# Performance work log

Measured on AMD Instinct MI355X. Metric: run time of the kernel, lower is better.

Reference implementation:

```python
import jax, jax.numpy as jnp
import numpy as np
from jax import lax

N, T, H = 16, 2048, 512


def setup_inputs() -> dict:
    key = jax.random.key(0)
    ks = jax.random.split(key, 4)
    scale = 0.02  # keep gates/tanh out of hard saturation
    return {
        "x": jax.random.normal(ks[0], (N, T, H), dtype=jnp.float32),
        "hidden": jnp.zeros((N, H), dtype=jnp.float32),
        "Wq": jax.random.normal(ks[1], (H, 2 * H), dtype=jnp.float32) * scale,
        "bq": jnp.zeros((H,), dtype=jnp.float32),
        "Wk": jax.random.normal(ks[2], (H, 2 * H), dtype=jnp.float32) * scale,
        "bk": jnp.zeros((H,), dtype=jnp.float32),
        "Wv": jax.random.normal(ks[3], (H, 2 * H), dtype=jnp.float32) * scale,
        "bv": jnp.zeros((H,), dtype=jnp.float32),
    }


def reference(x, hidden, Wq, bq, Wk, bk, Wv, bv):
    # x: (N, T, H); hidden: (N, H). torch Linear: y = cat @ W.T + b
    def step(h, xt):
        cat = jnp.concatenate([xt, h], axis=-1)  # (N, 2H)
        q = cat @ Wq.T + bq
        k = cat @ Wk.T + bk
        v = cat @ Wv.T + bv
        w = jax.nn.sigmoid(q * k)
        h_new = (1.0 - w) * h + w * jnp.tanh(v)
        return h_new, h  # emit PRE-update hidden (matches torch append-before-update)

    xs = jnp.swapaxes(x, 0, 1)  # (T, N, H)
    h_final, hiddens = lax.scan(step, hidden, xs)
    return jnp.swapaxes(hiddens, 0, 1), h_final  # (N, T, H), (N, H)
```

## Files before the change

### kernel.cpp

```cpp
#include <hip/hip_runtime.h>

#define N_B 16
#define T_S 2048
#define H_D 512
#define TH_F ((size_t)T_S * H_D)
#define NTH ((size_t)N_B * TH_F)
#define NGROUP 8
#define WPG 32
#define THREADS 512

#define STASH(dst, src) asm volatile("v_accvgpr_write_b32 %0, %1" : "=a"(dst) : "v"(src))
#define FETCH(dst, src) asm volatile("v_accvgpr_read_b32 %0, %1" : "=v"(dst) : "a"(src))

__global__ __launch_bounds__(THREADS, 1) void rnn_persist(
    const float* __restrict__ x,
    const float* __restrict__ hidden,
    const float* __restrict__ Wq, const float* __restrict__ bq,
    const float* __restrict__ Wk, const float* __restrict__ bk,
    const float* __restrict__ Wv, const float* __restrict__ bv,
    float* __restrict__ out,
    int* __restrict__ cnt)
{
    const int tid  = threadIdx.x;
    const int lane = tid & 63;
    const int wv   = tid >> 6;
    const int g    = blockIdx.x & 7;
    const int wm   = blockIdx.x >> 3;
    const int b0 = 2 * g, b1 = 2 * g + 1;
    const int jA = wm * 16 + 2 * wv;

    __shared__ __align__(16) float hs[2][H_D];

    float awx[2][3][8], awh[2][3][8];
    #pragma unroll
    for (int r = 0; r < 2; ++r) {
        const int j = jA + r;
        #pragma unroll
        for (int m = 0; m < 3; ++m) {
            const float* W = (m == 0) ? Wq : (m == 1) ? Wk : Wv;
            const float* base = W + (size_t)j * 1024 + lane * 8;
            float4 x0 = *(const float4*)(base);
            float4 x1 = *(const float4*)(base + 4);
            float4 h0 = *(const float4*)(base + 512);
            float4 h1 = *(const float4*)(base + 516);
            STASH(awx[r][m][0], x0.x); STASH(awx[r][m][1], x0.y);
            STASH(awx[r][m][2], x0.z); STASH(awx[r][m][3], x0.w);
            STASH(awx[r][m][4], x1.x); STASH(awx[r][m][5], x1.y);
            STASH(awx[r][m][6], x1.z); STASH(awx[r][m][7], x1.w);
            STASH(awh[r][m][0], h0.x); STASH(awh[r][m][1], h0.y);
            STASH(awh[r][m][2], h0.z); STASH(awh[r][m][3], h0.w);
            STASH(awh[r][m][4], h1.x); STASH(awh[r][m][5], h1.y);
            STASH(awh[r][m][6], h1.z); STASH(awh[r][m][7], h1.w);
        }
    }

    const int jw = jA + ((lane >> 1) & 1);
    const int bw = (lane & 1) ? b1 : b0;
    const float bqw = bq[jw], bkw = bk[jw], bvw = bv[jw];
    float ho = hidden[bw * H_D + jw];

    const int h_nb  = tid >> 8;
    const int u     = tid & 255;
    const int h_pos = u * 2;
    const int h_b   = h_nb ? b1 : b0;

    {
        float v0 = hidden[h_b * H_D + h_pos];
        float v1 = hidden[h_b * H_D + h_pos + 1];
        *(float2*)&hs[h_nb][h_pos] = make_float2(v0, v1);
        if (wm == 0) {
            out[(size_t)h_b * TH_F + h_pos]     = v0;
            out[(size_t)h_b * TH_F + h_pos + 1] = v1;
        }
    }
    __syncthreads();

    const float4* xb0 = (const float4*)(x + (size_t)b0 * TH_F) + lane * 2;
    const float4* xb1 = (const float4*)(x + (size_t)b1 * TH_F) + lane * 2;
    float ax[2][8];
    {
        float4 a = xb0[0], b = xb0[1], c = xb1[0], d = xb1[1];
        ax[0][0]=a.x; ax[0][1]=a.y; ax[0][2]=a.z; ax[0][3]=a.w;
        ax[0][4]=b.x; ax[0][5]=b.y; ax[0][6]=b.z; ax[0][7]=b.w;
        ax[1][0]=c.x; ax[1][1]=c.y; ax[1][2]=c.z; ax[1][3]=c.w;
        ax[1][4]=d.x; ax[1][5]=d.y; ax[1][6]=d.z; ax[1][7]=d.w;
    }

    int* mycnt = cnt + g * 64;

    for (int t = 0; t < T_S; ++t) {
        const bool do_next = (t + 1 < T_S);

        float acc[2][3][2];
        #pragma unroll
        for (int r = 0; r < 2; ++r)
            #pragma unroll
            for (int m = 0; m < 3; ++m) {
                float wreg[8];
                #pragma unroll
                for (int c = 0; c < 8; ++c) FETCH(wreg[c], awx[r][m][c]);
                float s0 = 0.f, s1 = 0.f;
                #pragma unroll
                for (int c = 0; c < 8; ++c) {
                    s0 = fmaf(wreg[c], ax[0][c], s0);
                    s1 = fmaf(wreg[c], ax[1][c], s1);
                }
                acc[r][m][0] = s0; acc[r][m][1] = s1;
            }

        if (do_next) {
            const size_t o = (size_t)(t + 1) * 128;
            float4 a = xb0[o], b = xb0[o + 1], c = xb1[o], d = xb1[o + 1];
            ax[0][0]=a.x; ax[0][1]=a.y; ax[0][2]=a.z; ax[0][3]=a.w;
            ax[0][4]=b.x; ax[0][5]=b.y; ax[0][6]=b.z; ax[0][7]=b.w;
            ax[1][0]=c.x; ax[1][1]=c.y; ax[1][2]=c.z; ax[1][3]=c.w;
            ax[1][4]=d.x; ax[1][5]=d.y; ax[1][6]=d.z; ax[1][7]=d.w;
        }

        if (t > 0) {
            if (tid == 0) {
                const int target = WPG * t;
                while (__hip_atomic_load(mycnt, __ATOMIC_RELAXED,
                                         __HIP_MEMORY_SCOPE_AGENT) < target) {}
            }
            __syncthreads();
            const unsigned long long* hsrc =
                (const unsigned long long*)(out + (size_t)h_b * TH_F + (size_t)t * H_D) + u;
            unsigned long long raw =
                __hip_atomic_load(hsrc, __ATOMIC_RELAXED, __HIP_MEMORY_SCOPE_AGENT);
            union { unsigned long long q; float2 f; } cv; cv.q = raw;
            *(float2*)&hs[h_nb][h_pos] = cv.f;
            __syncthreads();
        }

        float hbv[2][8];
        #pragma unroll
        for (int nb = 0; nb < 2; ++nb) {
            const float4* hp = (const float4*)&hs[nb][0] + lane * 2;
            float4 a0 = hp[0], a1 = hp[1];
            hbv[nb][0]=a0.x; hbv[nb][1]=a0.y; hbv[nb][2]=a0.z; hbv[nb][3]=a0.w;
            hbv[nb][4]=a1.x; hbv[nb][5]=a1.y; hbv[nb][6]=a1.z; hbv[nb][7]=a1.w;
        }
        #pragma unroll
        for (int r = 0; r < 2; ++r)
            #pragma unroll
            for (int m = 0; m < 3; ++m) {
                float wreg[8];
                #pragma unroll
                for (int c = 0; c < 8; ++c) FETCH(wreg[c], awh[r][m][c]);
                float s0 = acc[r][m][0], s1 = acc[r][m][1];
                #pragma unroll
                for (int c = 0; c < 8; ++c) {
                    s0 = fmaf(wreg[c], hbv[0][c], s0);
                    s1 = fmaf(wreg[c], hbv[1][c], s1);
                }
                acc[r][m][0] = s0; acc[r][m][1] = s1;
            }

        const bool lb0 = (lane & 1) != 0;
        const bool lb1 = (lane & 2) != 0;
        float a6[2][3];
        #pragma unroll
        for (int r = 0; r < 2; ++r)
            #pragma unroll
            for (int m = 0; m < 3; ++m) {
                float keep = lb0 ? acc[r][m][1] : acc[r][m][0];
                float send = lb0 ? acc[r][m][0] : acc[r][m][1];
                a6[r][m] = keep + __shfl_xor(send, 1);
            }
        float a3[3];
        #pragma unroll
        for (int m = 0; m < 3; ++m) {
            float keep = lb1 ? a6[1][m] : a6[0][m];
            float send = lb1 ? a6[0][m] : a6[1][m];
            a3[m] = keep + __shfl_xor(send, 2);
        }
        #pragma unroll
        for (int s = 4; s < 64; s <<= 1) {
            a3[0] += __shfl_xor(a3[0], s);
            a3[1] += __shfl_xor(a3[1], s);
            a3[2] += __shfl_xor(a3[2], s);
        }

        if (lane < 4) {
            const float q = a3[0] + bqw;
            const float k = a3[1] + bkw;
            const float v = a3[2] + bvw;
            const float e  = __expf(-q * k);
            const float w  = __builtin_amdgcn_rcpf(1.f + e);
            const float ev = __expf(2.f * v);
            const float th = 1.f - 2.f * __builtin_amdgcn_rcpf(ev + 1.f);
            const float hn = fmaf(w, th - ho, ho);
            const size_t opos = do_next
                ? ((size_t)bw * TH_F + (size_t)(t + 1) * H_D + jw)
                : (NTH + (size_t)bw * H_D + jw);
            __hip_atomic_store(out + opos, hn, __ATOMIC_RELAXED,
                               __HIP_MEMORY_SCOPE_AGENT);
            ho = hn;
        }

        __syncthreads();
        if (do_next && tid == 0)
            __hip_atomic_fetch_add(mycnt, 1, __ATOMIC_RELAXED,
                                   __HIP_MEMORY_SCOPE_AGENT);
    }
}

extern "C" void kernel_launch(void* const* d_in, const int* in_sizes, int n_in,
                              void* d_out, int out_size, void* d_ws, size_t ws_size,
                              hipStream_t stream) {
    const float* x      = (const float*)d_in[0];
    const float* hidden = (const float*)d_in[1];
    const float* Wq     = (const float*)d_in[2];
    const float* bq     = (const float*)d_in[3];
    const float* Wk     = (const float*)d_in[4];
    const float* bk     = (const float*)d_in[5];
    const float* Wv     = (const float*)d_in[6];
    const float* bv     = (const float*)d_in[7];
    float* out = (float*)d_out;
    int*   cnt = (int*)d_ws;

    hipMemsetAsync(cnt, 0, 16 * 64 * sizeof(int), stream);

    void* args[] = { (void*)&x, (void*)&hidden,
                     (void*)&Wq, (void*)&bq, (void*)&Wk, (void*)&bk,
                     (void*)&Wv, (void*)&bv, (void*)&out, (void*)&cnt };
    hipLaunchCooperativeKernel((const void*)rnn_persist,
                               dim3(NGROUP * WPG), dim3(THREADS),
                               args, 0, stream);
}
```

Measured before the change: 4.488 ms.

## Replace counter barrier with step-tagged hidden-state exchange buffers

Drops the per-group atomic counter barrier, along with its trailing syncthreads and fetch_add. Each new hidden value is now published as a 64-bit word that packs the timestep tag with the float, written into a double-buffered exchange area. Consumer threads spin directly on their own two words until the tags match, which removes a global round trip and one block barrier per step. It also double-buffers the shared hidden array so one syncthreads per step is enough. The cost is more polling traffic and an extra store per output, and correctness now depends on tag parity and buffer reuse across steps.

```diff
diff --git a/kernel.cpp b/kernel.cpp
--- a/kernel.cpp
+++ b/kernel.cpp
@@ -8,6 +8,8 @@
 #define NGROUP 8
 #define WPG 32
 #define THREADS 512
+#define EXG 1024
+#define EXP_W (NGROUP * EXG)
 
 #define STASH(dst, src) asm volatile("v_accvgpr_write_b32 %0, %1" : "=a"(dst) : "v"(src))
 #define FETCH(dst, src) asm volatile("v_accvgpr_read_b32 %0, %1" : "=v"(dst) : "a"(src))
@@ -19,7 +21,7 @@
     const float* __restrict__ Wk, const float* __restrict__ bk,
     const float* __restrict__ Wv, const float* __restrict__ bv,
     float* __restrict__ out,
-    int* __restrict__ cnt)
+    unsigned long long* __restrict__ ex)
 {
     const int tid  = threadIdx.x;
     const int lane = tid & 63;
@@ -29,7 +31,7 @@
     const int b0 = 2 * g, b1 = 2 * g + 1;
     const int jA = wm * 16 + 2 * wv;
 
-    __shared__ __align__(16) float hs[2][H_D];
+    __shared__ __align__(16) float hs[2][2][H_D];
 
     float awx[2][3][8], awh[2][3][8];
     #pragma unroll
@@ -60,14 +62,19 @@
     float ho = hidden[bw * H_D + jw];
 
     const int h_nb  = tid >> 8;
-    const int u     = tid & 255;
-    const int h_pos = u * 2;
+    const int h_pos = (tid & 255) * 2;
     const int h_b   = h_nb ? b1 : b0;
+
+    unsigned long long* const exg0 = ex + (size_t)g * EXG;
+    unsigned long long* const exg1 = exg0 + EXP_W;
+    unsigned long long* const sp0_p0 = exg0 + (size_t)tid * 2;
+    unsigned long long* const sp0_p1 = exg1 + (size_t)tid * 2;
+    const int exw_idx = (lane & 1) * 512 + jw;
 
     {
         float v0 = hidden[h_b * H_D + h_pos];
         float v1 = hidden[h_b * H_D + h_pos + 1];
-        *(float2*)&hs[h_nb][h_pos] = make_float2(v0, v1);
+        *(float2*)&hs[0][h_nb][h_pos] = make_float2(v0, v1);
         if (wm == 0) {
             out[(size_t)h_b * TH_F + h_pos]     = v0;
             out[(size_t)h_b * TH_F + h_pos + 1] = v1;
@@ -86,10 +93,16 @@
         ax[1][4]=d.x; ax[1][5]=d.y; ax[1][6]=d.z; ax[1][7]=d.w;
     }
 
-    int* mycnt = cnt + g * 64;
-
     for (int t = 0; t < T_S; ++t) {
         const bool do_next = (t + 1 < T_S);
+        const int  p  = t & 1;
+        unsigned long long* const spA = p ? sp0_p1 : sp0_p0;
+
+        unsigned long long w0 = 0, w1 = 0;
+        if (t > 0) {
+            w0 = __hip_atomic_load(spA,     __ATOMIC_RELAXED, __HIP_MEMORY_SCOPE_AGENT);
+            w1 = __hip_atomic_load(spA + 1, __ATOMIC_RELAXED, __HIP_MEMORY_SCOPE_AGENT);
+        }
 
         float acc[2][3][2];
         #pragma unroll
@@ -118,25 +131,22 @@
         }
 
         if (t > 0) {
-            if (tid == 0) {
-                const int target = WPG * t;
-                while (__hip_atomic_load(mycnt, __ATOMIC_RELAXED,
-                                         __HIP_MEMORY_SCOPE_AGENT) < target) {}
-            }
+            const unsigned tt = (unsigned)t;
+            while ((((unsigned)(w0 >> 32)) != tt) |
+                   (((unsigned)(w1 >> 32)) != tt)) {
+                w0 = __hip_atomic_load(spA,     __ATOMIC_RELAXED, __HIP_MEMORY_SCOPE_AGENT);
+                w1 = __hip_atomic_load(spA + 1, __ATOMIC_RELAXED, __HIP_MEMORY_SCOPE_AGENT);
+            }
+            union { unsigned u; float f; } c0, c1;
+            c0.u = (unsigned)w0; c1.u = (unsigned)w1;
+            *(float2*)&hs[p][h_nb][h_pos] = make_float2(c0.f, c1.f);
             __syncthreads();
-            const unsigned long long* hsrc =
-                (const unsigned long long*)(out + (size_t)h_b * TH_F + (size_t)t * H_D) + u;
-            unsigned long long raw =
-                __hip_atomic_load(hsrc, __ATOMIC_RELAXED, __HIP_MEMORY_SCOPE_AGENT);
-            union { unsigned long long q; float2 f; } cv; cv.q = raw;
-            *(float2*)&hs[h_nb][h_pos] = cv.f;
-            __syncthreads();
         }
 
         float hbv[2][8];
         #pragma unroll
         for (int nb = 0; nb < 2; ++nb) {
-            const float4* hp = (const float4*)&hs[nb][0] + lane * 2;
+            const float4* hp = (const float4*)&hs[p][nb][0] + lane * 2;
             float4 a0 = hp[0], a1 = hp[1];
             hbv[nb][0]=a0.x; hbv[nb][1]=a0.y; hbv[nb][2]=a0.z; hbv[nb][3]=a0.w;
             hbv[nb][4]=a1.x; hbv[nb][5]=a1.y; hbv[nb][6]=a1.z; hbv[nb][7]=a1.w;
@@ -191,18 +201,19 @@
             const float ev = __expf(2.f * v);
             const float th = 1.f - 2.f * __builtin_amdgcn_rcpf(ev + 1.f);
             const float hn = fmaf(w, th - ho, ho);
-            const size_t opos = do_next
-                ? ((size_t)bw * TH_F + (size_t)(t + 1) * H_D + jw)
-                : (NTH + (size_t)bw * H_D + jw);
-            __hip_atomic_store(out + opos, hn, __ATOMIC_RELAXED,
-                               __HIP_MEMORY_SCOPE_AGENT);
+            if (do_next) {
+                out[(size_t)bw * TH_F + (size_t)(t + 1) * H_D + jw] = hn;
+                union { float f; unsigned u; } cv; cv.f = hn;
+                unsigned long long* exwP = ((t + 1) & 1) ? (exg1 + exw_idx)
+                                                         : (exg0 + exw_idx);
+                __hip_atomic_store(exwP,
+                    (((unsigned long long)(unsigned)(t + 1)) << 32) | cv.u,
+                    __ATOMIC_RELAXED, __HIP_MEMORY_SCOPE_AGENT);
+            } else {
+                out[NTH + (size_t)bw * H_D + jw] = hn;
+            }
             ho = hn;
         }
-
-        __syncthreads();
-        if (do_next && tid == 0)
-            __hip_atomic_fetch_add(mycnt, 1, __ATOMIC_RELAXED,
-                                   __HIP_MEMORY_SCOPE_AGENT);
     }
 }
 
@@ -218,13 +229,13 @@
     const float* Wv     = (const float*)d_in[6];
     const float* bv     = (const float*)d_in[7];
     float* out = (float*)d_out;
-    int*   cnt = (int*)d_ws;
-
-    hipMemsetAsync(cnt, 0, 16 * 64 * sizeof(int), stream);
+    unsigned long long* ex = (unsigned long long*)d_ws;
+
+    hipMemsetAsync(ex, 0, 2 * EXP_W * sizeof(unsigned long long), stream);
 
     void* args[] = { (void*)&x, (void*)&hidden,
                      (void*)&Wq, (void*)&bq, (void*)&Wk, (void*)&bk,
-                     (void*)&Wv, (void*)&bv, (void*)&out, (void*)&cnt };
+                     (void*)&Wv, (void*)&bv, (void*)&out, (void*)&ex };
     hipLaunchCooperativeKernel((const void*)rnn_persist,
                                dim3(NGROUP * WPG), dim3(THREADS),
                                args, 0, stream);
```

Measured after the change: 4.806 ms. +7.1%, slower.
